# Kernel optimization log

Measured on AMD Instinct MI355X. Metric: run time of the kernel, lower is better.

## Reference

```python
import jax, jax.numpy as jnp
import numpy as np

LAGS = 2
SLOPE = 0.01  # nn.LeakyReLU default negative_slope


def setup_inputs() -> dict:
    key = jax.random.key(0)
    k0, k1, k2, k3, k4 = jax.random.split(key, 5)
    B, T, D, H = 64, 514, 32, 128
    IN = LAGS * D + 1
    x = jax.random.normal(k0, (B, T, D), dtype=jnp.float32)
    # per-latent-dim 2-layer MLP params (num_layers=3, layer_norm=False collapses to 2 Linears)
    W1 = jax.random.normal(k1, (D, H, IN), dtype=jnp.float32) / np.sqrt(IN).astype(np.float32)
    b1 = jax.random.normal(k2, (D, H), dtype=jnp.float32) * 0.01
    W2 = jax.random.normal(k3, (D, H), dtype=jnp.float32) / np.sqrt(H).astype(np.float32)
    b2 = jax.random.normal(k4, (D,), dtype=jnp.float32) * 0.01
    return {"x": x, "W1": W1, "b1": b1, "W2": W2, "b2": b2}


def reference(x, W1, b1, W2, b2):
    L = LAGS
    B, T, D = x.shape
    # unfold(dim=1, size=L+1, step=1) + swapaxes -> windows [B, T-L, L+1, D]
    idx = jnp.arange(T - L)[:, None] + jnp.arange(L + 1)[None, :]
    w = x[:, idx]                       # [B, T-L, L+1, D]
    w = w.reshape(-1, L + 1, D)         # [N, L+1, D]
    yy = w[:, -1, :]                    # [N, D]  current step, per dim
    xx = w[:, :-1, :].reshape(-1, L * D)  # [N, L*D] lagged history (shared)
    # batched tiny-MLP forward: input to g_i is [xx, yy[:, i]]
    pre = (jnp.einsum('nk,dhk->ndh', xx, W1[:, :, :-1])
           + yy[:, :, None] * W1[:, :, -1][None]
           + b1[None])                  # [N, D, H]
    act = jnp.where(pre >= 0, pre, SLOPE * pre)
    residuals = jnp.einsum('ndh,dh->nd', act, W2) + b2[None]  # [N, D]
    # analytic Jacobian of scalar output wrt the (L*D+1)-dim input:
    # J = (W2 * leaky'(pre)) @ W1
    dact = jnp.where(pre >= 0, jnp.float32(1.0), jnp.float32(SLOPE))
    g = dact * W2[None]                 # [N, D, H]
    jac = jnp.einsum('ndh,dhk->ndk', g, W1)  # [N, D, L*D+1]
    logabsdet = jnp.sum(jnp.log(jnp.abs(jac[:, :, -1])), axis=1)  # [N] summed over dims
    # hist_jac: torch returns a list of D tensors [N, 1, L*D]; stacked here as [D, N, 1, L*D]
    hist_jac = jnp.transpose(jac[:, :, :-1], (1, 0, 2))[:, :, None, :]
    residuals = residuals.reshape(B, T - L, D)
    sum_log_abs_det_jacobian = logabsdet.reshape(B, T - L).sum(axis=1)  # [B]
    return residuals, sum_log_abs_det_jacobian, hist_jac
```

## Files before the change

kernel.cpp:

```cpp
#include <hip/hip_runtime.h>
#include <math.h>


typedef _Float16 f16;
typedef __attribute__((ext_vector_type(8))) _Float16 half8;
typedef __attribute__((ext_vector_type(4))) _Float16 half4;
typedef __attribute__((ext_vector_type(4))) float floatx4;

namespace {
constexpr size_t W1F_SZ    = (size_t)32 * 8192 * 2;
constexpr size_t WS_W1F_HI = 0;
constexpr size_t WS_W1F_LO = W1F_SZ;
constexpr size_t WS_W1TF   = 2 * W1F_SZ;
constexpr size_t WS_EP     = 3 * W1F_SZ;
constexpr size_t WS_RES    = WS_EP + (size_t)32 * 128 * 16;

constexpr int XS_ROW = 40;
constexpr int GB_HP  = 136;

constexpr int L_GB   = 0;
constexpr int L_XSHI = 17408;
constexpr int L_XSLO = L_XSHI + 5280;
constexpr int L_YY   = L_XSLO + 5280;
constexpr int L_RES  = L_YY + 256;
constexpr int L_JAC  = L_RES + 1024;
constexpr int L_TOTAL = L_JAC + 1024;

constexpr size_t OUT1_OFF = (size_t)64 * 512 * 32;
constexpr size_t OUT2_OFF = OUT1_OFF + 64;
}

__global__ __launch_bounds__(256) void split_w1_kernel(
    const float* __restrict__ W1, const float* __restrict__ b1,
    const float* __restrict__ W2,
    f16* __restrict__ wh, f16* __restrict__ wl,
    f16* __restrict__ wT, float4* __restrict__ ep)
{
    int idx = blockIdx.x * 256 + threadIdx.x;
    if (idx >= 32 * 128 * 64) return;
    int d = idx >> 13, rem = idx & 8191;
    int h = rem >> 6, k = rem & 63;
    float v = W1[((size_t)(d * 128 + h)) * 65 + k];
    f16 hi = (f16)v;
    float r = v - (float)hi;
    int lane1 = (((k >> 3) & 3) << 4) | (h & 15);
    size_t o1 = ((((size_t)d * 8 + (h >> 4)) * 2 + (k >> 5)) * 64 + lane1) * 8 + (k & 7);
    wh[o1] = hi;
    wl[o1] = (f16)(r * 4096.0f);
    int lane2 = (((h >> 3) & 3) << 4) | (k & 15);
    size_t o2 = ((((size_t)d * 4 + (h >> 5)) * 4 + (k >> 4)) * 64 + lane2) * 8 + (h & 7);
    wT[o2] = hi;
    if (k == 63) {
        int hh = d * 128 + h;
        float w2 = W2[hh];
        float4 e;
        e.x = b1[hh];
        e.y = w2;
        e.z = 0.01f * w2;
        e.w = W1[(size_t)hh * 65 + 64];
        ep[hh] = e;
    }
}

__global__ __launch_bounds__(256, 4) void np_main_kernel(
    const float* __restrict__ x,
    const float* __restrict__ b2,
    const char* __restrict__ ws,
    float* __restrict__ resw,
    float* __restrict__ out)
{
    extern __shared__ char smem[];
    const int tile = blockIdx.x;
    const int d    = blockIdx.y;
    const int b    = tile >> 3;
    const int t0   = (tile & 7) << 6;
    const int tid  = threadIdx.x;
    const int wave = tid >> 6, lane = tid & 63;
    const int c = lane & 15, q = lane >> 4;

    float* yyL  = (float*)(smem + L_YY);
    float* resP = (float*)(smem + L_RES);
    float* jacP = (float*)(smem + L_JAC);

    const f16* w1fh = (const f16*)(ws + WS_W1F_HI) + (size_t)d * 8192;
    const f16* w1fl = (const f16*)(ws + WS_W1F_LO) + (size_t)d * 8192;
    const f16* w1tf = (const f16*)(ws + WS_W1TF)   + (size_t)d * 8192;
    const float4* epd = (const float4*)(ws + WS_EP) + d * 128;

    {
        const float4* xs = (const float4*)(x + (size_t)(b * 514 + t0) * 32);
        for (int u = tid; u < 528; u += 256) {
            float4 v = xs[u];
            int row = u >> 3, c4 = u & 7;
            half4 hi, lo;
            #pragma unroll
            for (int j = 0; j < 4; ++j) {
                float vv = (&v.x)[j];
                f16 h = (f16)vv;
                hi[j] = h;
                lo[j] = (f16)((vv - (float)h) * 4096.0f);
            }
            *(half4*)(smem + L_XSHI + (row * XS_ROW + c4 * 4) * 2) = hi;
            *(half4*)(smem + L_XSLO + (row * XS_ROW + c4 * 4) * 2) = lo;
        }
        if (tid < 64) yyL[tid] = x[(size_t)(b * 514 + t0 + tid + 2) * 32 + d];
    }
    __syncthreads();

    float yyv[4];
    #pragma unroll
    for (int nt = 0; nt < 4; ++nt) yyv[nt] = yyL[nt * 16 + c];

    float res[4] = {0.f, 0.f, 0.f, 0.f}, j64[4] = {0.f, 0.f, 0.f, 0.f};

    #pragma unroll
    for (int ht = 0; ht < 2; ++ht) {
        const int hbase = wave * 32 + ht * 16 + q * 4;

        float4 epv[4];
        #pragma unroll
        for (int r = 0; r < 4; ++r) epv[r] = epd[hbase + r];

        floatx4 accP[4], accQ[4];
        #pragma unroll
        for (int nt = 0; nt < 4; ++nt) { accP[nt] = (floatx4)0.f; accQ[nt] = (floatx4)0.f; }

        #pragma unroll
        for (int ks = 0; ks < 2; ++ks) {
            const int fo = (((wave * 2 + ht) * 2 + ks) * 64 + lane) * 8;
            const half8 aH = *(const half8*)(w1fh + fo);
            const half8 aL = *(const half8*)(w1fl + fo);
            half8 bH[4], bL[4];
            #pragma unroll
            for (int nt = 0; nt < 4; ++nt) {
                const int off = (nt * 16 + c + ks) * XS_ROW + q * 8;
                bH[nt] = *(const half8*)(smem + L_XSHI + off * 2);
                bL[nt] = *(const half8*)(smem + L_XSLO + off * 2);
            }
            #pragma unroll
            for (int nt = 0; nt < 4; ++nt) {
                accP[nt] = __builtin_amdgcn_mfma_f32_16x16x32_f16(aH, bH[nt], accP[nt], 0, 0, 0);
                accQ[nt] = __builtin_amdgcn_mfma_f32_16x16x32_f16(aH, bL[nt], accQ[nt], 0, 0, 0);
                accQ[nt] = __builtin_amdgcn_mfma_f32_16x16x32_f16(aL, bH[nt], accQ[nt], 0, 0, 0);
            }
        }

        #pragma unroll
        for (int nt = 0; nt < 4; ++nt) {
            const int n = nt * 16 + c;
            half4 gp;
            #pragma unroll
            for (int r = 0; r < 4; ++r) {
                const float pre = accP[nt][r] + accQ[nt][r] * (1.0f / 4096.0f)
                                + epv[r].x + yyv[nt] * epv[r].w;
                const float gg = (pre >= 0.f) ? epv[r].y : epv[r].z;
                res[nt] += pre * gg;
                j64[nt] += gg * epv[r].w;
                gp[r] = (f16)gg;
            }
            *(half4*)(smem + L_GB + (n * GB_HP + hbase) * 2) = gp;
        }
    }

    #pragma unroll
    for (int nt = 0; nt < 4; ++nt) {
        float rv = res[nt];
        rv += __shfl_xor(rv, 16, 64);
        rv += __shfl_xor(rv, 32, 64);
        float jv = j64[nt];
        jv += __shfl_xor(jv, 16, 64);
        jv += __shfl_xor(jv, 32, 64);
        if (lane < 16) {
            resP[wave * 64 + nt * 16 + lane] = rv;
            jacP[wave * 64 + nt * 16 + lane] = jv;
        }
    }
    __syncthreads();

    if (tid < 64) {
        const int n = tid;
        float r = b2[d], j = 0.f;
        #pragma unroll
        for (int w = 0; w < 4; ++w) { r += resP[w * 64 + n]; j += jacP[w * 64 + n]; }
        resw[(size_t)d * 32768 + (size_t)(b * 512 + t0) + n] = r;
        float lg = logf(fabsf(j));
        #pragma unroll
        for (int off = 32; off > 0; off >>= 1) lg += __shfl_down(lg, off, 64);
        if (tid == 0) atomicAdd(out + OUT1_OFF + b, lg);
    }

    floatx4 acc2[4];
    #pragma unroll
    for (int kt = 0; kt < 4; ++kt) acc2[kt] = (floatx4)0.f;
    #pragma unroll
    for (int ks = 0; ks < 4; ++ks) {
        const half8 gF = *(const half8*)(smem + L_GB + ((wave * 16 + c) * GB_HP + ks * 32 + q * 8) * 2);
        #pragma unroll
        for (int kt = 0; kt < 4; ++kt) {
            const half8 wF = *(const half8*)(w1tf + ((ks * 4 + kt) * 64 + lane) * 8);
            acc2[kt] = __builtin_amdgcn_mfma_f32_16x16x32_f16(wF, gF, acc2[kt], 0, 0, 0);
        }
    }
    {
        float* out2 = out + OUT2_OFF + (size_t)d * ((size_t)32768 * 64)
                    + (size_t)(b * 512 + t0 + wave * 16) * 64;
        #pragma unroll
        for (int kt = 0; kt < 4; ++kt)
            *(floatx4*)(out2 + (size_t)c * 64 + kt * 16 + q * 4) = acc2[kt];
    }
}

__global__ __launch_bounds__(256) void finish_res_kernel(
    const float* __restrict__ resw, float* __restrict__ out)
{
    __shared__ float tile[32][65];
    const int n0 = blockIdx.x * 64;
    const int tid = threadIdx.x;
    #pragma unroll
    for (int i = 0; i < 8; ++i) {
        int idx = i * 256 + tid;
        int dd = idx >> 6, n = idx & 63;
        tile[dd][n] = resw[(size_t)dd * 32768 + n0 + n];
    }
    __syncthreads();
    #pragma unroll
    for (int i = 0; i < 8; ++i) {
        int idx = i * 256 + tid;
        int n = idx >> 5, dd = idx & 31;
        out[(size_t)(n0 + n) * 32 + dd] = tile[dd][n];
    }
}

extern "C" void kernel_launch(void* const* d_in, const int* in_sizes, int n_in,
                              void* d_out, int out_size, void* d_ws, size_t ws_size,
                              hipStream_t stream) {
    const float* x  = (const float*)d_in[0];
    const float* W1 = (const float*)d_in[1];
    const float* b1 = (const float*)d_in[2];
    const float* W2 = (const float*)d_in[3];
    const float* b2 = (const float*)d_in[4];
    float* out = (float*)d_out;
    char* ws = (char*)d_ws;

    hipMemsetAsync(out + OUT1_OFF, 0, 64 * sizeof(float), stream);

    hipLaunchKernelGGL(split_w1_kernel, dim3((32 * 128 * 64 + 255) / 256), dim3(256), 0, stream,
                       W1, b1, W2, (f16*)(ws + WS_W1F_HI), (f16*)(ws + WS_W1F_LO),
                       (f16*)(ws + WS_W1TF), (float4*)(ws + WS_EP));

    hipLaunchKernelGGL(np_main_kernel, dim3(512, 32), dim3(256), L_TOTAL, stream,
                       x, b2, (const char*)ws, (float*)(ws + WS_RES), out);

    hipLaunchKernelGGL(finish_res_kernel, dim3(512), dim3(256), 0, stream,
                       (const float*)(ws + WS_RES), out);
}
```

Measured before the change: 372.0 us.

## Pre-split x into fp16 hi/lo once and write residuals directly

```diff
diff --git a/kernel.cpp b/kernel.cpp
--- a/kernel.cpp
+++ b/kernel.cpp
@@ -8,14 +8,16 @@
 typedef __attribute__((ext_vector_type(4))) float floatx4;
 
 namespace {
-constexpr size_t W1F_SZ    = (size_t)32 * 8192 * 2;
-constexpr size_t WS_W1F_HI = 0;
-constexpr size_t WS_W1F_LO = W1F_SZ;
-constexpr size_t WS_W1TF   = 2 * W1F_SZ;
-constexpr size_t WS_EP     = 3 * W1F_SZ;
-constexpr size_t WS_RES    = WS_EP + (size_t)32 * 128 * 16;
-
-constexpr int XS_ROW = 40;
+constexpr int    XS_ROW   = 40;
+constexpr size_t XS_SPLIT = (size_t)64 * 514 * XS_ROW * 2;
+constexpr size_t WS_XS_HI = 0;
+constexpr size_t WS_XS_LO = XS_SPLIT;
+constexpr size_t W1F_SZ   = (size_t)32 * 8192 * 2;
+constexpr size_t WS_W1F_HI = 2 * XS_SPLIT;
+constexpr size_t WS_W1F_LO = WS_W1F_HI + W1F_SZ;
+constexpr size_t WS_W1TF   = WS_W1F_LO + W1F_SZ;
+constexpr size_t WS_EP     = WS_W1TF + W1F_SZ;
+
 constexpr int GB_HP  = 136;
 
 constexpr int L_GB   = 0;
@@ -28,6 +30,19 @@
 
 constexpr size_t OUT1_OFF = (size_t)64 * 512 * 32;
 constexpr size_t OUT2_OFF = OUT1_OFF + 64;
+}
+
+__global__ __launch_bounds__(256) void split_x_kernel(
+    const float* __restrict__ x, f16* __restrict__ xh, f16* __restrict__ xl)
+{
+    int idx = blockIdx.x * 256 + threadIdx.x;
+    if (idx >= 64 * 514 * 32) return;
+    int row = idx >> 5, c = idx & 31;
+    float v = x[idx];
+    f16 hi = (f16)v;
+    float r = v - (float)hi;
+    xh[row * XS_ROW + c] = hi;
+    xl[row * XS_ROW + c] = (f16)(r * 4096.0f);
 }
 
 __global__ __launch_bounds__(256) void split_w1_kernel(
@@ -66,7 +81,6 @@
     const float* __restrict__ x,
     const float* __restrict__ b2,
     const char* __restrict__ ws,
-    float* __restrict__ resw,
     float* __restrict__ out)
 {
     extern __shared__ char smem[];
@@ -88,21 +102,11 @@
     const float4* epd = (const float4*)(ws + WS_EP) + d * 128;
 
     {
-        const float4* xs = (const float4*)(x + (size_t)(b * 514 + t0) * 32);
-        for (int u = tid; u < 528; u += 256) {
-            float4 v = xs[u];
-            int row = u >> 3, c4 = u & 7;
-            half4 hi, lo;
-            #pragma unroll
-            for (int j = 0; j < 4; ++j) {
-                float vv = (&v.x)[j];
-                f16 h = (f16)vv;
-                hi[j] = h;
-                lo[j] = (f16)((vv - (float)h) * 4096.0f);
-            }
-            *(half4*)(smem + L_XSHI + (row * XS_ROW + c4 * 4) * 2) = hi;
-            *(half4*)(smem + L_XSLO + (row * XS_ROW + c4 * 4) * 2) = lo;
-        }
+        const float4* s3 = (const float4*)(ws + WS_XS_HI + (size_t)(b * 514 + t0) * (XS_ROW * 2));
+        const float4* s4 = (const float4*)(ws + WS_XS_LO + (size_t)(b * 514 + t0) * (XS_ROW * 2));
+        float4* d3 = (float4*)(smem + L_XSHI);
+        float4* d4 = (float4*)(smem + L_XSLO);
+        for (int i = tid; i < 330; i += 256) { d3[i] = s3[i]; d4[i] = s4[i]; }
         if (tid < 64) yyL[tid] = x[(size_t)(b * 514 + t0 + tid + 2) * 32 + d];
     }
     __syncthreads();
@@ -182,7 +186,7 @@
         float r = b2[d], j = 0.f;
         #pragma unroll
         for (int w = 0; w < 4; ++w) { r += resP[w * 64 + n]; j += jacP[w * 64 + n]; }
-        resw[(size_t)d * 32768 + (size_t)(b * 512 + t0) + n] = r;
+        out[(size_t)(b * 512 + t0 + n) * 32 + d] = r;
         float lg = logf(fabsf(j));
         #pragma unroll
         for (int off = 32; off > 0; off >>= 1) lg += __shfl_down(lg, off, 64);
@@ -207,27 +211,6 @@
         #pragma unroll
         for (int kt = 0; kt < 4; ++kt)
             *(floatx4*)(out2 + (size_t)c * 64 + kt * 16 + q * 4) = acc2[kt];
-    }
-}
-
-__global__ __launch_bounds__(256) void finish_res_kernel(
-    const float* __restrict__ resw, float* __restrict__ out)
-{
-    __shared__ float tile[32][65];
-    const int n0 = blockIdx.x * 64;
-    const int tid = threadIdx.x;
-    #pragma unroll
-    for (int i = 0; i < 8; ++i) {
-        int idx = i * 256 + tid;
-        int dd = idx >> 6, n = idx & 63;
-        tile[dd][n] = resw[(size_t)dd * 32768 + n0 + n];
-    }
-    __syncthreads();
-    #pragma unroll
-    for (int i = 0; i < 8; ++i) {
-        int idx = i * 256 + tid;
-        int n = idx >> 5, dd = idx & 31;
-        out[(size_t)(n0 + n) * 32 + dd] = tile[dd][n];
     }
 }
 
@@ -244,13 +227,12 @@
 
     hipMemsetAsync(out + OUT1_OFF, 0, 64 * sizeof(float), stream);
 
+    hipLaunchKernelGGL(split_x_kernel, dim3((64 * 514 * 32 + 255) / 256), dim3(256), 0, stream,
+                       x, (f16*)(ws + WS_XS_HI), (f16*)(ws + WS_XS_LO));
     hipLaunchKernelGGL(split_w1_kernel, dim3((32 * 128 * 64 + 255) / 256), dim3(256), 0, stream,
                        W1, b1, W2, (f16*)(ws + WS_W1F_HI), (f16*)(ws + WS_W1F_LO),
                        (f16*)(ws + WS_W1TF), (float4*)(ws + WS_EP));
 
     hipLaunchKernelGGL(np_main_kernel, dim3(512, 32), dim3(256), L_TOTAL, stream,
-                       x, b2, (const char*)ws, (float*)(ws + WS_RES), out);
-
-    hipLaunchKernelGGL(finish_res_kernel, dim3(512), dim3(256), 0, stream,
-                       (const float*)(ws + WS_RES), out);
-}
+                       x, b2, (const char*)ws, out);
+}
```

Measured after the change: 378.7 us. About the same (+1.8%).
